# Optimization experiments

Hardware: AMD Instinct MI355X
Metric: run time of the kernel (lower is better)

Reference implementation:

```python
import jax, jax.numpy as jnp
import numpy as np

NUM_HEADS = 4
SPATIAL_DS = 2
EPS = 1e-5


def setup_inputs() -> dict:
    key = jax.random.key(0)
    ks = jax.random.split(key, 6)
    B, C, H, W = 8, 256, 64, 64
    hd = C // NUM_HEADS
    return {
        "x": jax.random.normal(ks[0], (B, C, H, W), jnp.float32),
        "gn_w": jnp.ones((C,), jnp.float32),
        "gn_b": jnp.zeros((C,), jnp.float32),
        "wq": jax.random.normal(ks[1], (C, C), jnp.float32) * (C ** -0.5),
        "wk": jax.random.normal(ks[2], (hd, C), jnp.float32) * (C ** -0.5),
        "wv": jax.random.normal(ks[3], (hd, C), jnp.float32) * (C ** -0.5),
        "wo": jax.random.normal(ks[4], (C, C), jnp.float32) * (C ** -0.5),
        "gamma": jnp.full((C,), 1e-4, jnp.float32),
    }


def reference(x, gn_w, gn_b, wq, wk, wv, wo, gamma):
    B, C, H, W = x.shape
    hd = C // NUM_HEADS
    scale = hd ** -0.5
    ds = SPATIAL_DS

    # GroupNorm with 1 group: normalize over (C,H,W) per sample, per-channel affine
    mu = jnp.mean(x, axis=(1, 2, 3), keepdims=True)
    var = jnp.var(x, axis=(1, 2, 3), keepdims=True)
    xn = (x - mu) * jax.lax.rsqrt(var + EPS)
    xn = xn * gn_w[None, :, None, None] + gn_b[None, :, None, None]

    # Q projection (1x1 conv == channel matmul): (B, heads, N, hd)
    q = jnp.einsum('oc,bchw->bohw', wq, xn).reshape(B, NUM_HEADS, hd, H * W)
    q = jnp.swapaxes(q, 2, 3)  # (B, h, N, hd)

    # AvgPool2d(ds, ds) on normalized input for K/V
    Hd, Wd = H // ds, W // ds
    x_ds = xn.reshape(B, C, Hd, ds, Wd, ds).mean(axis=(3, 5))

    k = jnp.einsum('oc,bchw->bohw', wk, x_ds).reshape(B, hd, Hd * Wd)
    k = jnp.swapaxes(k, 1, 2)  # (B, M, hd) single shared head
    v = jnp.einsum('oc,bchw->bohw', wv, x_ds).reshape(B, hd, Hd * Wd)
    v = jnp.swapaxes(v, 1, 2)  # (B, M, hd)

    # Multi-query attention: queries per-head, shared K/V
    attn = jnp.einsum('bhnd,bmd->bhnm', q, k) * scale
    attn = jax.nn.softmax(attn, axis=-1)
    out = jnp.einsum('bhnm,bmd->bhnd', attn, v)  # (B, h, N, hd)

    out = jnp.swapaxes(out, 2, 3).reshape(B, C, H, W)
    out = jnp.einsum('oc,bchw->bohw', wo, out)

    return x + out * gamma[None, :, None, None]
```

## Files before the change

kernel.cpp:

```cpp
#include <hip/hip_runtime.h>


#define CNT_INV (1.0f/1048576.0f)
#define EPSV 1e-5f
#define QSCALE 0.18033688f

#define WS_STATS 0
#define WS_XNT   64
#define WS_XDS   4194368
#define WS_K     5242944
#define WS_V     5505088
#define WS_WQB   5767232
#define WS_WKV   5800000
#define WS_WOB   5816384

typedef __attribute__((ext_vector_type(8))) short bf8_t;
typedef __attribute__((ext_vector_type(4))) float f4_t;

static __device__ __forceinline__ unsigned fbits(float f) {
  union { float f; unsigned u; } v; v.f = f; return v.u;
}
static __device__ __forceinline__ unsigned short f2bf(float f) {
  unsigned u = fbits(f);
  return (unsigned short)((u + 0x7fffu + ((u >> 16) & 1u)) >> 16);
}
static __device__ __forceinline__ unsigned pk_rnd(float a, float b) {
  return __builtin_amdgcn_perm(fbits(b) + 0x8000u, fbits(a) + 0x8000u, 0x07060302u);
}
static __device__ __forceinline__ unsigned pk_tr(float a, float b) {
  return __builtin_amdgcn_perm(fbits(b), fbits(a), 0x07060302u);
}
static __device__ __forceinline__ float bf2f(unsigned short h) {
  union { unsigned u; float f; } v; v.u = ((unsigned)h) << 16; return v.f;
}
static __device__ __forceinline__ float fexp2(float x) {
  float r; asm("v_exp_f32 %0, %1" : "=v"(r) : "v"(x)); return r;
}

__global__ __launch_bounds__(256) void k_prep_stats(const float* __restrict__ x,
                                                    const float* __restrict__ wq,
                                                    const float* __restrict__ wk,
                                                    const float* __restrict__ wv,
                                                    const float* __restrict__ wo,
                                                    float* __restrict__ stats,
                                                    unsigned short* __restrict__ wqb,
                                                    unsigned short* __restrict__ wkvb,
                                                    unsigned short* __restrict__ wob) {
  const int blk = blockIdx.x;
  const int t = threadIdx.x;
  if (blk < 512) {
    const int b = blk >> 6;
    const int chunk = blk & 63;
    const float4* xb = (const float4*)(x + (size_t)b * 1048576 + (size_t)chunk * 16384);
    float s = 0.f, s2 = 0.f;
#pragma unroll
    for (int it = 0; it < 16; ++it) {
      float4 v = xb[it * 256 + t];
      s  += v.x + v.y + v.z + v.w;
      s2 += v.x * v.x + v.y * v.y + v.z * v.z + v.w * v.w;
    }
#pragma unroll
    for (int o = 32; o > 0; o >>= 1) {
      s  += __shfl_down(s, o);
      s2 += __shfl_down(s2, o);
    }
    __shared__ float red[8];
    const int wid = t >> 6;
    if ((t & 63) == 0) { red[wid] = s; red[4 + wid] = s2; }
    __syncthreads();
    if (t == 0) {
      atomicAdd(&stats[b * 2 + 0], red[0] + red[1] + red[2] + red[3]);
      atomicAdd(&stats[b * 2 + 1], red[4] + red[5] + red[6] + red[7]);
    }
  } else {
    const int idx = (blk - 512) * 256 + t;
    if (idx < 65536) wqb[idx] = f2bf(wq[idx]);
    else if (idx < 81920) wkvb[idx - 65536] = f2bf(wk[idx - 65536]);
    else if (idx < 98304) wkvb[idx - 65536] = f2bf(wv[idx - 81920]);
    else if (idx < 163840) wob[idx - 98304] = f2bf(wo[idx - 98304]);
  }
}

__global__ __launch_bounds__(256) void k_xnt(const float* __restrict__ x,
                                             const float* __restrict__ gnw,
                                             const float* __restrict__ gnb,
                                             const float* __restrict__ stats,
                                             unsigned short* __restrict__ xnT,
                                             unsigned short* __restrict__ xdsT) {
  __shared__ unsigned short T[128][72];
  const int t = threadIdx.x;
  const int b = blockIdx.z, c0 = blockIdx.y * 64, hp = blockIdx.x;
  const int n0 = hp * 128;
  const float mu = stats[b * 2 + 0] * CNT_INV;
  const float rstd = rsqrtf(stats[b * 2 + 1] * CNT_INV - mu * mu + EPSV);
  const int n4 = (t & 31) * 4, cl = t >> 5;
  const int wswz = t & 7;
#pragma unroll
  for (int p = 0; p < 8; ++p) {
    const int c = c0 + p * 8 + cl;
    const float gw = gnw[c] * rstd;
    const float gb = gnb[c] - mu * rstd * gnw[c];
    const int pc = (p ^ wswz) * 8 + cl;
    float4 v = *(const float4*)&x[(size_t)(b * 256 + c) * 4096 + n0 + n4];
    T[n4 + 0][pc] = f2bf(v.x * gw + gb);
    T[n4 + 1][pc] = f2bf(v.y * gw + gb);
    T[n4 + 2][pc] = f2bf(v.z * gw + gb);
    T[n4 + 3][pc] = f2bf(v.w * gw + gb);
  }
  __syncthreads();
  {
    const int r = t >> 1, cb4 = (t & 1) * 4;
    const int rswz = (t >> 3) & 7;
    unsigned short* dst = xnT + ((size_t)b * 4096 + n0 + r) * 256 + c0 + cb4 * 8;
#pragma unroll
    for (int u = 0; u < 4; ++u)
      *(uint4*)(dst + u * 8) = *(const uint4*)&T[r][((cb4 + u) ^ rswz) * 8];
  }
  {
    const int wd = t >> 3, c8 = t & 7;
    const int pswz = (wd >> 1) & 7;
    const int pc = (c8 ^ pswz) * 8;
    uint4 u0 = *(const uint4*)&T[2 * wd][pc];
    uint4 u1 = *(const uint4*)&T[2 * wd + 1][pc];
    uint4 u2 = *(const uint4*)&T[64 + 2 * wd][pc];
    uint4 u3 = *(const uint4*)&T[64 + 2 * wd + 1][pc];
    const unsigned* p0 = (const unsigned*)&u0; const unsigned* p1 = (const unsigned*)&u1;
    const unsigned* p2 = (const unsigned*)&u2; const unsigned* p3 = (const unsigned*)&u3;
    unsigned outp[4];
#pragma unroll
    for (int i = 0; i < 4; ++i) {
      float lo = (bf2f((unsigned short)p0[i]) + bf2f((unsigned short)p1[i]) +
                  bf2f((unsigned short)p2[i]) + bf2f((unsigned short)p3[i])) * 0.25f;
      float hi = (bf2f((unsigned short)(p0[i] >> 16)) + bf2f((unsigned short)(p1[i] >> 16)) +
                  bf2f((unsigned short)(p2[i] >> 16)) + bf2f((unsigned short)(p3[i] >> 16))) * 0.25f;
      outp[i] = pk_rnd(lo, hi);
    }
    *(uint4*)(xdsT + ((size_t)b * 1024 + hp * 32 + wd) * 256 + c0 + c8 * 8) = *(uint4*)outp;
  }
}

__global__ __launch_bounds__(256) void k_gemm_kv(const unsigned short* __restrict__ wkvb,
                                                 const unsigned short* __restrict__ xdsT,
                                                 unsigned short* __restrict__ kbf,
                                                 unsigned short* __restrict__ vtbf) {
  __shared__ __align__(16) unsigned short kv[2][64][72];
  const int t = threadIdx.x;
  const int w = t >> 6, l = t & 63, lane16 = l & 15, quad = l >> 4;
  const int m0 = blockIdx.x * 64, b = blockIdx.y;
  const unsigned short* Abase = wkvb + (size_t)(w * 32 + lane16) * 256 + quad * 8;
  const unsigned short* Bbase = xdsT + ((size_t)b * 1024 + m0 + lane16) * 256 + quad * 8;
  f4_t acc[2][4];
#pragma unroll
  for (int i = 0; i < 2; ++i)
#pragma unroll
    for (int j = 0; j < 4; ++j) acc[i][j] = (f4_t){0.f, 0.f, 0.f, 0.f};
  bf8_t Ac[2], Bc[4];
#pragma unroll
  for (int og = 0; og < 2; ++og) Ac[og] = *(const bf8_t*)(Abase + (size_t)og * 16 * 256);
#pragma unroll
  for (int mg = 0; mg < 4; ++mg) Bc[mg] = *(const bf8_t*)(Bbase + (size_t)mg * 16 * 256);
  for (int kc = 0; kc < 256; kc += 32) {
    const int kn = (kc + 32) & 255;
    bf8_t An[2], Bn[4];
#pragma unroll
    for (int og = 0; og < 2; ++og) An[og] = *(const bf8_t*)(Abase + (size_t)og * 16 * 256 + kn);
#pragma unroll
    for (int mg = 0; mg < 4; ++mg) Bn[mg] = *(const bf8_t*)(Bbase + (size_t)mg * 16 * 256 + kn);
#pragma unroll
    for (int og = 0; og < 2; ++og)
#pragma unroll
      for (int mg = 0; mg < 4; ++mg)
        acc[og][mg] = __builtin_amdgcn_mfma_f32_16x16x32_bf16(Ac[og], Bc[mg], acc[og][mg], 0, 0, 0);
#pragma unroll
    for (int og = 0; og < 2; ++og) Ac[og] = An[og];
#pragma unroll
    for (int mg = 0; mg < 4; ++mg) Bc[mg] = Bn[mg];
  }
  if (w < 2) {
#pragma unroll
    for (int og = 0; og < 2; ++og)
#pragma unroll
      for (int mg = 0; mg < 4; ++mg) {
        uint2 p;
        p.x = pk_rnd(acc[og][mg][0], acc[og][mg][1]);
        p.y = pk_rnd(acc[og][mg][2], acc[og][mg][3]);
        *(uint2*)&kv[0][mg * 16 + lane16][w * 32 + og * 16 + quad * 4] = p;
      }
  } else {
#pragma unroll
    for (int og = 0; og < 2; ++og)
#pragma unroll
      for (int mg = 0; mg < 4; ++mg) {
        const int d0 = (w - 2) * 32 + og * 16 + quad * 4;
#pragma unroll
        for (int r = 0; r < 4; ++r)
          kv[1][d0 + r][mg * 16 + lane16] = f2bf(acc[og][mg][r]);
      }
  }
  __syncthreads();
  {
    const int row = t >> 2, q2 = t & 3;
    const int e = row & 7;
    uint4 k0 = *(const uint4*)&kv[0][row][q2 * 16];
    uint4 k1 = *(const uint4*)&kv[0][row][q2 * 16 + 8];
    unsigned short* kd = kbf + (size_t)b * 65536 + (size_t)(m0 + row) * 64;
    *(uint4*)(kd + ((q2 * 2) ^ e) * 8)     = k0;
    *(uint4*)(kd + ((q2 * 2 + 1) ^ e) * 8) = k1;
    uint4 v0 = *(const uint4*)&kv[1][row][q2 * 16];
    uint4 v1 = *(const uint4*)&kv[1][row][q2 * 16 + 8];
    unsigned short* vd = vtbf + (size_t)b * 65536 + (size_t)(blockIdx.x * 2 + (q2 >> 1)) * 2048 +
                         (size_t)row * 32 + (q2 & 1) * 16;
    *(uint4*)vd = v0; *(uint4*)(vd + 8) = v1;
  }
}

__global__ __launch_bounds__(256) void k_fused(const unsigned short* __restrict__ wqb,
                                               const unsigned short* __restrict__ xnT,
                                               const unsigned short* __restrict__ kbf,
                                               const unsigned short* __restrict__ vtbf,
                                               const unsigned short* __restrict__ wob,
                                               const float* __restrict__ x,
                                               const float* __restrict__ gamma,
                                               float* __restrict__ outp) {
  __shared__ __align__(16) unsigned short smem[20480];
  __shared__ __align__(16) unsigned short kst[2][2048];
  __shared__ __align__(16) unsigned short vst[2][2048];
  const int t = threadIdx.x;
  const int w = t >> 6, l = t & 63, lane16 = l & 15, quad = l >> 4;
  const int n0 = blockIdx.x * 64, b = blockIdx.y;
  const int h = w;
  unsigned short* qst = smem + w * 4608;
  unsigned short (*plds)[64][40] = (unsigned short (*)[64][40])(smem + w * 5120);
  unsigned short (*aos)[264] = (unsigned short (*)[264])smem;

  const int sw = w & 1;
  const unsigned short* sbase = (w < 2) ? (kbf + (size_t)b * 65536) : (vtbf + (size_t)b * 65536);
  unsigned short* sdst0 = ((w < 2) ? &kst[0][0] : &vst[0][0]) + sw * 1024 + l * 8;
  unsigned short* sdst1 = ((w < 2) ? &kst[1][0] : &vst[1][0]) + sw * 1024 + l * 8;

#define STAGE_ISSUE(WIN, R0, R1)                                              \
  { const unsigned short* sp = sbase + (size_t)(WIN) * 2048 + sw * 1024 + l * 8; \
    R0 = *(const uint4*)sp; R1 = *(const uint4*)(sp + 512); }
#define STAGE_WRITE(DP, R0, R1)                                               \
  { *(uint4*)(DP) = R0; *(uint4*)((DP) + 512) = R1; }

#define READ_K(BUF, KREG)                                                     \
  {                                                                           \
    _Pragma("unroll")                                                         \
    for (int s = 0; s < 2; ++s) {                                             \
      _Pragma("unroll")                                                       \
      for (int dc = 0; dc < 2; ++dc)                                          \
        KREG[s][dc] = *(const bf8_t*)&kst[BUF][(s * 16 + lane16) * 64 +       \
                                              (((dc * 4 + quad) ^ (lane16 & 7)) * 8)]; \
    }                                                                         \
  }
#define READ_V(BUF, VREG)                                                     \
  {                                                                           \
    _Pragma("unroll")                                                         \
    for (int dg = 0; dg < 4; ++dg)                                            \
      VREG[dg] = *(const bf8_t*)&vst[BUF][(dg * 16 + lane16) * 32 + quad * 8]; \
  }

  const unsigned short* kb = kbf;

  {
    const unsigned short* Abase = wqb + (size_t)(h * 64 + lane16) * 256 + quad * 8;
    const unsigned short* Bbase = xnT + ((size_t)b * 4096 + n0 + lane16) * 256 + quad * 8;
    f4_t qacc[4][4];
#pragma unroll
    for (int i = 0; i < 4; ++i)
#pragma unroll
      for (int j = 0; j < 4; ++j) qacc[i][j] = (f4_t){0.f, 0.f, 0.f, 0.f};
    for (int kc = 0; kc < 256; kc += 32) {
      bf8_t A[4], Bf[4];
#pragma unroll
      for (int og = 0; og < 4; ++og) A[og] = *(const bf8_t*)(Abase + (size_t)og * 16 * 256 + kc);
#pragma unroll
      for (int ng = 0; ng < 4; ++ng) Bf[ng] = *(const bf8_t*)(Bbase + (size_t)ng * 16 * 256 + kc);
#pragma unroll
      for (int og = 0; og < 4; ++og)
#pragma unroll
        for (int ng = 0; ng < 4; ++ng)
          qacc[og][ng] = __builtin_amdgcn_mfma_f32_16x16x32_bf16(A[og], Bf[ng], qacc[og][ng], 0, 0, 0);
    }
#pragma unroll
    for (int og = 0; og < 4; ++og)
#pragma unroll
      for (int ng = 0; ng < 4; ++ng) {
        uint2 p;
        p.x = pk_rnd(qacc[og][ng][0] * QSCALE, qacc[og][ng][1] * QSCALE);
        p.y = pk_rnd(qacc[og][ng][2] * QSCALE, qacc[og][ng][3] * QSCALE);
        *(uint2*)&qst[(ng * 16 + lane16) * 72 + og * 16 + quad * 4] = p;
      }
  }
  bf8_t Qf[4][2];
#pragma unroll
  for (int qg = 0; qg < 4; ++qg)
#pragma unroll
    for (int dc = 0; dc < 2; ++dc)
      Qf[qg][dc] = *(const bf8_t*)&qst[(qg * 16 + lane16) * 72 + dc * 32 + quad * 8];
  __syncthreads();

  f4_t O[4][4];
#pragma unroll
  for (int dg = 0; dg < 4; ++dg)
#pragma unroll
    for (int qg = 0; qg < 4; ++qg) O[dg][qg] = (f4_t){0.f, 0.f, 0.f, 0.f};
  f4_t O4[4];
#pragma unroll
  for (int qg = 0; qg < 4; ++qg) O4[qg] = (f4_t){0.f, 0.f, 0.f, 0.f};
  const short onebf = (lane16 == 0) ? (short)0x3F80 : (short)0;
  const bf8_t Aone = {onebf, onebf, onebf, onebf, onebf, onebf, onebf, onebf};

#define SSTEP(KREG, BUF)                                                      \
  {                                                                           \
    _Pragma("unroll")                                                         \
    for (int qg = 0; qg < 4; ++qg) {                                          \
      _Pragma("unroll")                                                       \
      for (int s = 0; s < 2; ++s) {                                           \
        f4_t S = (f4_t){0.f, 0.f, 0.f, 0.f};                                  \
        S = __builtin_amdgcn_mfma_f32_16x16x32_bf16(KREG[s][0], Qf[qg][0], S, 0, 0, 0); \
        S = __builtin_amdgcn_mfma_f32_16x16x32_bf16(KREG[s][1], Qf[qg][1], S, 0, 0, 0); \
        float e0 = fexp2(S[0]);                                               \
        float e1 = fexp2(S[1]);                                               \
        float e2 = fexp2(S[2]);                                               \
        float e3 = fexp2(S[3]);                                               \
        uint2 p; p.x = pk_tr(e0, e1); p.y = pk_tr(e2, e3);                    \
        *(uint2*)&plds[BUF][qg * 16 + lane16][s * 16 + quad * 4] = p;         \
      }                                                                       \
    }                                                                         \
  }

  {
    uint4 a0, a1, b0, b1;
    STAGE_ISSUE(0, a0, a1);
    STAGE_ISSUE(1, b0, b1);
    STAGE_WRITE(sdst0, a0, a1);
    STAGE_WRITE(sdst1, b0, b1);
  }
  __syncthreads();

  bf8_t Kc[2][2], Vc[4];
  READ_K(0, Kc);
  SSTEP(Kc, 0);
  READ_V(0, Vc);
  __syncthreads();

  for (int it = 1; it < 32; ++it) {
    const int cur = it & 1, pb = cur ^ 1;
    uint4 g0, g1;
    if (it < 31) STAGE_ISSUE(it + 1, g0, g1);
    bf8_t Pf[4];
#pragma unroll
    for (int qg = 0; qg < 4; ++qg)
      Pf[qg] = *(const bf8_t*)&plds[pb][qg * 16 + lane16][quad * 8];
    READ_K(cur, Kc);
    bf8_t Vn[4];
    READ_V(cur, Vn);
    __builtin_amdgcn_s_setprio(1);
#pragma unroll
    for (int dg = 0; dg < 4; ++dg)
#pragma unroll
      for (int qg = 0; qg < 4; ++qg)
        O[dg][qg] = __builtin_amdgcn_mfma_f32_16x16x32_bf16(Vc[dg], Pf[qg], O[dg][qg], 0, 0, 0);
#pragma unroll
    for (int qg = 0; qg < 4; ++qg)
      O4[qg] = __builtin_amdgcn_mfma_f32_16x16x32_bf16(Aone, Pf[qg], O4[qg], 0, 0, 0);
    __builtin_amdgcn_s_setprio(0);
    SSTEP(Kc, cur);
#pragma unroll
    for (int dg = 0; dg < 4; ++dg) Vc[dg] = Vn[dg];
    if (it < 31) STAGE_WRITE((cur ? sdst0 : sdst1), g0, g1);
    __syncthreads();
  }
  {
    bf8_t Pf[4];
#pragma unroll
    for (int qg = 0; qg < 4; ++qg)
      Pf[qg] = *(const bf8_t*)&plds[1][qg * 16 + lane16][quad * 8];
    __builtin_amdgcn_s_setprio(1);
#pragma unroll
    for (int dg = 0; dg < 4; ++dg)
#pragma unroll
      for (int qg = 0; qg < 4; ++qg)
        O[dg][qg] = __builtin_amdgcn_mfma_f32_16x16x32_bf16(Vc[dg], Pf[qg], O[dg][qg], 0, 0, 0);
#pragma unroll
    for (int qg = 0; qg < 4; ++qg)
      O4[qg] = __builtin_amdgcn_mfma_f32_16x16x32_bf16(Aone, Pf[qg], O4[qg], 0, 0, 0);
    __builtin_amdgcn_s_setprio(0);
  }
#undef SSTEP
#undef STAGE_ISSUE
#undef STAGE_WRITE
#undef READ_K
#undef READ_V
  (void)kb;

  float rden[4];
#pragma unroll
  for (int qg = 0; qg < 4; ++qg) {
    float d = __shfl(O4[qg][0], lane16);
    rden[qg] = 1.f / d;
  }

  __syncthreads();
#pragma unroll
  for (int dg = 0; dg < 4; ++dg)
#pragma unroll
    for (int qg = 0; qg < 4; ++qg) {
      const int c0 = h * 64 + dg * 16 + quad * 4;
      uint2 p;
      p.x = pk_rnd(O[dg][qg][0] * rden[qg], O[dg][qg][1] * rden[qg]);
      p.y = pk_rnd(O[dg][qg][2] * rden[qg], O[dg][qg][3] * rden[qg]);
      *(uint2*)&aos[qg * 16 + lane16][c0] = p;
    }
  __syncthreads();

  {
    const unsigned short* Wbase = wob + (size_t)(w * 64 + lane16) * 256 + quad * 8;
    f4_t acc[4][4];
#pragma unroll
    for (int i = 0; i < 4; ++i)
#pragma unroll
      for (int j = 0; j < 4; ++j) acc[i][j] = (f4_t){0.f, 0.f, 0.f, 0.f};
    for (int kc = 0; kc < 256; kc += 32) {
      bf8_t A[4], Bf[4];
#pragma unroll
      for (int og = 0; og < 4; ++og) A[og] = *(const bf8_t*)(Wbase + (size_t)og * 16 * 256 + kc);
#pragma unroll
      for (int ng = 0; ng < 4; ++ng) Bf[ng] = *(const bf8_t*)&aos[ng * 16 + lane16][kc + quad * 8];
#pragma unroll
      for (int og = 0; og < 4; ++og)
#pragma unroll
        for (int ng = 0; ng < 4; ++ng)
          acc[og][ng] = __builtin_amdgcn_mfma_f32_16x16x32_bf16(A[og], Bf[ng], acc[og][ng], 0, 0, 0);
    }
#pragma unroll
    for (int og = 0; og < 4; ++og) {
      float4 g4 = *(const float4*)&gamma[w * 64 + og * 16 + quad * 4];
      const float g[4] = {g4.x, g4.y, g4.z, g4.w};
#pragma unroll
      for (int ng = 0; ng < 4; ++ng) {
        const int n = n0 + ng * 16 + lane16;
#pragma unroll
        for (int r = 0; r < 4; ++r) {
          const int o = w * 64 + og * 16 + quad * 4 + r;
          const size_t ix = ((size_t)(b * 256 + o)) * 4096 + n;
          outp[ix] = x[ix] + g[r] * acc[og][ng][r];
        }
      }
    }
  }
}

extern "C" void kernel_launch(void* const* d_in, const int* in_sizes, int n_in,
                              void* d_out, int out_size, void* d_ws, size_t ws_size,
                              hipStream_t stream) {
  const float* x     = (const float*)d_in[0];
  const float* gnw   = (const float*)d_in[1];
  const float* gnb   = (const float*)d_in[2];
  const float* wq    = (const float*)d_in[3];
  const float* wk    = (const float*)d_in[4];
  const float* wv    = (const float*)d_in[5];
  const float* wo    = (const float*)d_in[6];
  const float* gamma = (const float*)d_in[7];
  float* out = (float*)d_out;
  float* ws  = (float*)d_ws;
  unsigned short* xnT  = (unsigned short*)(ws + WS_XNT);
  unsigned short* xdsT = (unsigned short*)(ws + WS_XDS);
  unsigned short* kbf  = (unsigned short*)(ws + WS_K);
  unsigned short* vtbf = (unsigned short*)(ws + WS_V);
  unsigned short* wqb  = (unsigned short*)(ws + WS_WQB);
  unsigned short* wkvb = (unsigned short*)(ws + WS_WKV);
  unsigned short* wob  = (unsigned short*)(ws + WS_WOB);

  hipMemsetAsync(ws, 0, 256, stream);
  k_prep_stats<<<1152, 256, 0, stream>>>(x, wq, wk, wv, wo, ws + WS_STATS, wqb, wkvb, wob);
  k_xnt<<<dim3(32, 4, 8), 256, 0, stream>>>(x, gnw, gnb, ws + WS_STATS, xnT, xdsT);
  k_gemm_kv<<<dim3(16, 8), 256, 0, stream>>>(wkvb, xdsT, kbf, vtbf);
  k_fused<<<dim3(64, 8), 256, 0, stream>>>(wqb, xnT, kbf, vtbf, wob, x, gamma, out);
}
```

Before: 194.1 us.

## Split fused attention KV range across two wave groups with 512-thread blocks

The fused attention kernel now runs 8 waves per block. Two groups of four waves each handle half of the 1024 key/value positions for the same 64 queries, and the partial numerators and denominators are combined through shared memory before the output projection. The Q projection and the output projection are split across both groups as well. The software-pipelined softmax step (compute P for the next window while consuming the previous one) is replaced by a simpler sequential per-window loop, and the KV GEMM drops its register prefetch. This raises wave-level parallelism and shortens each wave's serial loop, at the cost of extra barriers, a shared-memory reduction and a less overlapped inner loop.

```diff
diff --git a/kernel.cpp b/kernel.cpp
--- a/kernel.cpp
+++ b/kernel.cpp
@@ -126,16 +126,16 @@
     uint4 u3 = *(const uint4*)&T[64 + 2 * wd + 1][pc];
     const unsigned* p0 = (const unsigned*)&u0; const unsigned* p1 = (const unsigned*)&u1;
     const unsigned* p2 = (const unsigned*)&u2; const unsigned* p3 = (const unsigned*)&u3;
-    unsigned outp[4];
+    unsigned outv[4];
 #pragma unroll
     for (int i = 0; i < 4; ++i) {
       float lo = (bf2f((unsigned short)p0[i]) + bf2f((unsigned short)p1[i]) +
                   bf2f((unsigned short)p2[i]) + bf2f((unsigned short)p3[i])) * 0.25f;
       float hi = (bf2f((unsigned short)(p0[i] >> 16)) + bf2f((unsigned short)(p1[i] >> 16)) +
                   bf2f((unsigned short)(p2[i] >> 16)) + bf2f((unsigned short)(p3[i] >> 16))) * 0.25f;
-      outp[i] = pk_rnd(lo, hi);
-    }
-    *(uint4*)(xdsT + ((size_t)b * 1024 + hp * 32 + wd) * 256 + c0 + c8 * 8) = *(uint4*)outp;
+      outv[i] = pk_rnd(lo, hi);
+    }
+    *(uint4*)(xdsT + ((size_t)b * 1024 + hp * 32 + wd) * 256 + c0 + c8 * 8) = *(uint4*)outv;
   }
 }
 
@@ -154,27 +154,17 @@
   for (int i = 0; i < 2; ++i)
 #pragma unroll
     for (int j = 0; j < 4; ++j) acc[i][j] = (f4_t){0.f, 0.f, 0.f, 0.f};
-  bf8_t Ac[2], Bc[4];
-#pragma unroll
-  for (int og = 0; og < 2; ++og) Ac[og] = *(const bf8_t*)(Abase + (size_t)og * 16 * 256);
-#pragma unroll
-  for (int mg = 0; mg < 4; ++mg) Bc[mg] = *(const bf8_t*)(Bbase + (size_t)mg * 16 * 256);
   for (int kc = 0; kc < 256; kc += 32) {
-    const int kn = (kc + 32) & 255;
-    bf8_t An[2], Bn[4];
-#pragma unroll
-    for (int og = 0; og < 2; ++og) An[og] = *(const bf8_t*)(Abase + (size_t)og * 16 * 256 + kn);
-#pragma unroll
-    for (int mg = 0; mg < 4; ++mg) Bn[mg] = *(const bf8_t*)(Bbase + (size_t)mg * 16 * 256 + kn);
+    bf8_t A[2], Bf[4];
+#pragma unroll
+    for (int og = 0; og < 2; ++og) A[og] = *(const bf8_t*)(Abase + (size_t)og * 16 * 256 + kc);
+#pragma unroll
+    for (int mg = 0; mg < 4; ++mg) Bf[mg] = *(const bf8_t*)(Bbase + (size_t)mg * 16 * 256 + kc);
 #pragma unroll
     for (int og = 0; og < 2; ++og)
 #pragma unroll
       for (int mg = 0; mg < 4; ++mg)
-        acc[og][mg] = __builtin_amdgcn_mfma_f32_16x16x32_bf16(Ac[og], Bc[mg], acc[og][mg], 0, 0, 0);
-#pragma unroll
-    for (int og = 0; og < 2; ++og) Ac[og] = An[og];
-#pragma unroll
-    for (int mg = 0; mg < 4; ++mg) Bc[mg] = Bn[mg];
+        acc[og][mg] = __builtin_amdgcn_mfma_f32_16x16x32_bf16(A[og], Bf[mg], acc[og][mg], 0, 0, 0);
   }
   if (w < 2) {
 #pragma unroll
@@ -214,43 +204,84 @@
   }
 }
 
-__global__ __launch_bounds__(256) void k_fused(const unsigned short* __restrict__ wqb,
-                                               const unsigned short* __restrict__ xnT,
-                                               const unsigned short* __restrict__ kbf,
-                                               const unsigned short* __restrict__ vtbf,
-                                               const unsigned short* __restrict__ wob,
-                                               const float* __restrict__ x,
-                                               const float* __restrict__ gamma,
-                                               float* __restrict__ outp) {
-  __shared__ __align__(16) unsigned short smem[20480];
-  __shared__ __align__(16) unsigned short kst[2][2048];
-  __shared__ __align__(16) unsigned short vst[2][2048];
+__global__ __launch_bounds__(512, 4) void k_fused(const unsigned short* __restrict__ wqb,
+                                                  const unsigned short* __restrict__ xnT,
+                                                  const unsigned short* __restrict__ kbf,
+                                                  const unsigned short* __restrict__ vtbf,
+                                                  const unsigned short* __restrict__ wob,
+                                                  const float* __restrict__ x,
+                                                  const float* __restrict__ gamma,
+                                                  float* __restrict__ outp) {
+  __shared__ __align__(16) unsigned short smem[18432];
+  __shared__ __align__(16) unsigned short kstA[2][2][2048];
+  __shared__ __align__(16) unsigned short vstA[2][2][2048];
   const int t = threadIdx.x;
   const int w = t >> 6, l = t & 63, lane16 = l & 15, quad = l >> 4;
+  const int h = w & 3, kvg = w >> 2;
   const int n0 = blockIdx.x * 64, b = blockIdx.y;
-  const int h = w;
-  unsigned short* qst = smem + w * 4608;
-  unsigned short (*plds)[64][40] = (unsigned short (*)[64][40])(smem + w * 5120);
+  unsigned short* qst = smem + h * 4608;
+  unsigned short (*plds)[36] = (unsigned short (*)[36])(smem + w * 2304);
   unsigned short (*aos)[264] = (unsigned short (*)[264])smem;
 
-  const int sw = w & 1;
-  const unsigned short* sbase = (w < 2) ? (kbf + (size_t)b * 65536) : (vtbf + (size_t)b * 65536);
-  unsigned short* sdst0 = ((w < 2) ? &kst[0][0] : &vst[0][0]) + sw * 1024 + l * 8;
-  unsigned short* sdst1 = ((w < 2) ? &kst[1][0] : &vst[1][0]) + sw * 1024 + l * 8;
+  const unsigned short* kb = kbf + (size_t)b * 65536;
+  const unsigned short* vb = vtbf + (size_t)b * 65536;
+
+  {
+    const unsigned short* Abase = wqb + (size_t)(h * 64 + lane16) * 256 + quad * 8;
+    const unsigned short* Bbase = xnT + ((size_t)b * 4096 + n0 + kvg * 32 + lane16) * 256 + quad * 8;
+    f4_t qacc[4][2];
+#pragma unroll
+    for (int i = 0; i < 4; ++i)
+#pragma unroll
+      for (int j = 0; j < 2; ++j) qacc[i][j] = (f4_t){0.f, 0.f, 0.f, 0.f};
+    for (int kc = 0; kc < 256; kc += 32) {
+      bf8_t A[4], Bf[2];
+#pragma unroll
+      for (int og = 0; og < 4; ++og) A[og] = *(const bf8_t*)(Abase + (size_t)og * 16 * 256 + kc);
+#pragma unroll
+      for (int j = 0; j < 2; ++j) Bf[j] = *(const bf8_t*)(Bbase + (size_t)j * 16 * 256 + kc);
+#pragma unroll
+      for (int og = 0; og < 4; ++og)
+#pragma unroll
+        for (int j = 0; j < 2; ++j)
+          qacc[og][j] = __builtin_amdgcn_mfma_f32_16x16x32_bf16(A[og], Bf[j], qacc[og][j], 0, 0, 0);
+    }
+#pragma unroll
+    for (int og = 0; og < 4; ++og)
+#pragma unroll
+      for (int j = 0; j < 2; ++j) {
+        const int ng = kvg * 2 + j;
+        uint2 p;
+        p.x = pk_rnd(qacc[og][j][0] * QSCALE, qacc[og][j][1] * QSCALE);
+        p.y = pk_rnd(qacc[og][j][2] * QSCALE, qacc[og][j][3] * QSCALE);
+        *(uint2*)&qst[(ng * 16 + lane16) * 72 + og * 16 + quad * 4] = p;
+      }
+  }
+  __syncthreads();
+  bf8_t Qf[4][2];
+#pragma unroll
+  for (int qg = 0; qg < 4; ++qg)
+#pragma unroll
+    for (int dc = 0; dc < 2; ++dc)
+      Qf[qg][dc] = *(const bf8_t*)&qst[(qg * 16 + lane16) * 72 + dc * 32 + quad * 8];
+
+  const int wr = w & 3, sw = wr & 1;
+  const unsigned short* sbase = (wr < 2) ? kb : vb;
+  unsigned short* sdst0 = ((wr < 2) ? &kstA[kvg][0][0] : &vstA[kvg][0][0]) + sw * 1024 + l * 8;
+  unsigned short* sdst1 = ((wr < 2) ? &kstA[kvg][1][0] : &vstA[kvg][1][0]) + sw * 1024 + l * 8;
 
 #define STAGE_ISSUE(WIN, R0, R1)                                              \
   { const unsigned short* sp = sbase + (size_t)(WIN) * 2048 + sw * 1024 + l * 8; \
     R0 = *(const uint4*)sp; R1 = *(const uint4*)(sp + 512); }
 #define STAGE_WRITE(DP, R0, R1)                                               \
   { *(uint4*)(DP) = R0; *(uint4*)((DP) + 512) = R1; }
-
 #define READ_K(BUF, KREG)                                                     \
   {                                                                           \
     _Pragma("unroll")                                                         \
     for (int s = 0; s < 2; ++s) {                                             \
       _Pragma("unroll")                                                       \
       for (int dc = 0; dc < 2; ++dc)                                          \
-        KREG[s][dc] = *(const bf8_t*)&kst[BUF][(s * 16 + lane16) * 64 +       \
+        KREG[s][dc] = *(const bf8_t*)&kstA[kvg][BUF][(s * 16 + lane16) * 64 + \
                                               (((dc * 4 + quad) ^ (lane16 & 7)) * 8)]; \
     }                                                                         \
   }
@@ -258,47 +289,14 @@
   {                                                                           \
     _Pragma("unroll")                                                         \
     for (int dg = 0; dg < 4; ++dg)                                            \
-      VREG[dg] = *(const bf8_t*)&vst[BUF][(dg * 16 + lane16) * 32 + quad * 8]; \
-  }
-
-  const unsigned short* kb = kbf;
-
-  {
-    const unsigned short* Abase = wqb + (size_t)(h * 64 + lane16) * 256 + quad * 8;
-    const unsigned short* Bbase = xnT + ((size_t)b * 4096 + n0 + lane16) * 256 + quad * 8;
-    f4_t qacc[4][4];
-#pragma unroll
-    for (int i = 0; i < 4; ++i)
-#pragma unroll
-      for (int j = 0; j < 4; ++j) qacc[i][j] = (f4_t){0.f, 0.f, 0.f, 0.f};
-    for (int kc = 0; kc < 256; kc += 32) {
-      bf8_t A[4], Bf[4];
-#pragma unroll
-      for (int og = 0; og < 4; ++og) A[og] = *(const bf8_t*)(Abase + (size_t)og * 16 * 256 + kc);
-#pragma unroll
-      for (int ng = 0; ng < 4; ++ng) Bf[ng] = *(const bf8_t*)(Bbase + (size_t)ng * 16 * 256 + kc);
-#pragma unroll
-      for (int og = 0; og < 4; ++og)
-#pragma unroll
-        for (int ng = 0; ng < 4; ++ng)
-          qacc[og][ng] = __builtin_amdgcn_mfma_f32_16x16x32_bf16(A[og], Bf[ng], qacc[og][ng], 0, 0, 0);
-    }
-#pragma unroll
-    for (int og = 0; og < 4; ++og)
-#pragma unroll
-      for (int ng = 0; ng < 4; ++ng) {
-        uint2 p;
-        p.x = pk_rnd(qacc[og][ng][0] * QSCALE, qacc[og][ng][1] * QSCALE);
-        p.y = pk_rnd(qacc[og][ng][2] * QSCALE, qacc[og][ng][3] * QSCALE);
-        *(uint2*)&qst[(ng * 16 + lane16) * 72 + og * 16 + quad * 4] = p;
-      }
-  }
-  bf8_t Qf[4][2];
-#pragma unroll
-  for (int qg = 0; qg < 4; ++qg)
-#pragma unroll
-    for (int dc = 0; dc < 2; ++dc)
-      Qf[qg][dc] = *(const bf8_t*)&qst[(qg * 16 + lane16) * 72 + dc * 32 + quad * 8];
+      VREG[dg] = *(const bf8_t*)&vstA[kvg][BUF][(dg * 16 + lane16) * 32 + quad * 8]; \
+  }
+
+  {
+    uint4 a0, a1;
+    STAGE_ISSUE(kvg * 16, a0, a1);
+    STAGE_WRITE(sdst0, a0, a1);
+  }
   __syncthreads();
 
   f4_t O[4][4];
@@ -312,51 +310,33 @@
   const short onebf = (lane16 == 0) ? (short)0x3F80 : (short)0;
   const bf8_t Aone = {onebf, onebf, onebf, onebf, onebf, onebf, onebf, onebf};
 
-#define SSTEP(KREG, BUF)                                                      \
-  {                                                                           \
-    _Pragma("unroll")                                                         \
-    for (int qg = 0; qg < 4; ++qg) {                                          \
-      _Pragma("unroll")                                                       \
-      for (int s = 0; s < 2; ++s) {                                           \
-        f4_t S = (f4_t){0.f, 0.f, 0.f, 0.f};                                  \
-        S = __builtin_amdgcn_mfma_f32_16x16x32_bf16(KREG[s][0], Qf[qg][0], S, 0, 0, 0); \
-        S = __builtin_amdgcn_mfma_f32_16x16x32_bf16(KREG[s][1], Qf[qg][1], S, 0, 0, 0); \
-        float e0 = fexp2(S[0]);                                               \
-        float e1 = fexp2(S[1]);                                               \
-        float e2 = fexp2(S[2]);                                               \
-        float e3 = fexp2(S[3]);                                               \
-        uint2 p; p.x = pk_tr(e0, e1); p.y = pk_tr(e2, e3);                    \
-        *(uint2*)&plds[BUF][qg * 16 + lane16][s * 16 + quad * 4] = p;         \
-      }                                                                       \
-    }                                                                         \
-  }
-
-  {
-    uint4 a0, a1, b0, b1;
-    STAGE_ISSUE(0, a0, a1);
-    STAGE_ISSUE(1, b0, b1);
-    STAGE_WRITE(sdst0, a0, a1);
-    STAGE_WRITE(sdst1, b0, b1);
-  }
-  __syncthreads();
-
-  bf8_t Kc[2][2], Vc[4];
-  READ_K(0, Kc);
-  SSTEP(Kc, 0);
-  READ_V(0, Vc);
-  __syncthreads();
-
-  for (int it = 1; it < 32; ++it) {
-    const int cur = it & 1, pb = cur ^ 1;
+  for (int it = 0; it < 16; ++it) {
+    const int cur = it & 1;
     uint4 g0, g1;
-    if (it < 31) STAGE_ISSUE(it + 1, g0, g1);
+    if (it < 15) STAGE_ISSUE(kvg * 16 + it + 1, g0, g1);
+    bf8_t Kc[2][2];
+    READ_K(cur, Kc);
+#pragma unroll
+    for (int qg = 0; qg < 4; ++qg) {
+#pragma unroll
+      for (int s = 0; s < 2; ++s) {
+        f4_t S = (f4_t){0.f, 0.f, 0.f, 0.f};
+        S = __builtin_amdgcn_mfma_f32_16x16x32_bf16(Kc[s][0], Qf[qg][0], S, 0, 0, 0);
+        S = __builtin_amdgcn_mfma_f32_16x16x32_bf16(Kc[s][1], Qf[qg][1], S, 0, 0, 0);
+        float e0 = fexp2(S[0]);
+        float e1 = fexp2(S[1]);
+        float e2 = fexp2(S[2]);
+        float e3 = fexp2(S[3]);
+        uint2 p; p.x = pk_tr(e0, e1); p.y = pk_tr(e2, e3);
+        *(uint2*)&plds[qg * 16 + lane16][s * 16 + quad * 4] = p;
+      }
+    }
+    bf8_t Vc[4];
+    READ_V(cur, Vc);
     bf8_t Pf[4];
 #pragma unroll
     for (int qg = 0; qg < 4; ++qg)
-      Pf[qg] = *(const bf8_t*)&plds[pb][qg * 16 + lane16][quad * 8];
-    READ_K(cur, Kc);
-    bf8_t Vn[4];
-    READ_V(cur, Vn);
+      Pf[qg] = *(const bf8_t*)&plds[qg * 16 + lane16][quad * 8];
     __builtin_amdgcn_s_setprio(1);
 #pragma unroll
     for (int dg = 0; dg < 4; ++dg)
@@ -367,84 +347,100 @@
     for (int qg = 0; qg < 4; ++qg)
       O4[qg] = __builtin_amdgcn_mfma_f32_16x16x32_bf16(Aone, Pf[qg], O4[qg], 0, 0, 0);
     __builtin_amdgcn_s_setprio(0);
-    SSTEP(Kc, cur);
-#pragma unroll
-    for (int dg = 0; dg < 4; ++dg) Vc[dg] = Vn[dg];
-    if (it < 31) STAGE_WRITE((cur ? sdst0 : sdst1), g0, g1);
+    if (it < 15) STAGE_WRITE((cur ? sdst0 : sdst1), g0, g1);
     __syncthreads();
   }
-  {
-    bf8_t Pf[4];
-#pragma unroll
-    for (int qg = 0; qg < 4; ++qg)
-      Pf[qg] = *(const bf8_t*)&plds[1][qg * 16 + lane16][quad * 8];
-    __builtin_amdgcn_s_setprio(1);
-#pragma unroll
-    for (int dg = 0; dg < 4; ++dg)
-#pragma unroll
-      for (int qg = 0; qg < 4; ++qg)
-        O[dg][qg] = __builtin_amdgcn_mfma_f32_16x16x32_bf16(Vc[dg], Pf[qg], O[dg][qg], 0, 0, 0);
-#pragma unroll
-    for (int qg = 0; qg < 4; ++qg)
-      O4[qg] = __builtin_amdgcn_mfma_f32_16x16x32_bf16(Aone, Pf[qg], O4[qg], 0, 0, 0);
-    __builtin_amdgcn_s_setprio(0);
-  }
-#undef SSTEP
 #undef STAGE_ISSUE
 #undef STAGE_WRITE
 #undef READ_K
 #undef READ_V
-  (void)kb;
-
-  float rden[4];
-#pragma unroll
-  for (int qg = 0; qg < 4; ++qg) {
-    float d = __shfl(O4[qg][0], lane16);
-    rden[qg] = 1.f / d;
-  }
-
-  __syncthreads();
-#pragma unroll
-  for (int dg = 0; dg < 4; ++dg)
+
+  float* fcomb = (float*)&kstA[0][0][0];
+#pragma unroll
+  for (int dgr = 0; dgr < 4; ++dgr) {
+    if (kvg == 1) {
+#pragma unroll
+      for (int qg = 0; qg < 4; ++qg)
+#pragma unroll
+        for (int rr = 0; rr < 4; ++rr)
+          fcomb[(qg * 4 + rr) * 256 + h * 64 + l] = O[dgr][qg][rr];
+    }
+    __syncthreads();
+    if (kvg == 0) {
+#pragma unroll
+      for (int qg = 0; qg < 4; ++qg)
+#pragma unroll
+        for (int rr = 0; rr < 4; ++rr)
+          O[dgr][qg][rr] += fcomb[(qg * 4 + rr) * 256 + h * 64 + l];
+    }
+    __syncthreads();
+  }
+  if (kvg == 1) {
+#pragma unroll
+    for (int qg = 0; qg < 4; ++qg)
+#pragma unroll
+      for (int rr = 0; rr < 4; ++rr)
+        fcomb[(qg * 4 + rr) * 256 + h * 64 + l] = O4[qg][rr];
+  }
+  __syncthreads();
+  if (kvg == 0) {
+#pragma unroll
+    for (int qg = 0; qg < 4; ++qg)
+#pragma unroll
+      for (int rr = 0; rr < 4; ++rr)
+        O4[qg][rr] += fcomb[(qg * 4 + rr) * 256 + h * 64 + l];
+  }
+  __syncthreads();
+
+  if (kvg == 0) {
+    float rden[4];
 #pragma unroll
     for (int qg = 0; qg < 4; ++qg) {
-      const int c0 = h * 64 + dg * 16 + quad * 4;
-      uint2 p;
-      p.x = pk_rnd(O[dg][qg][0] * rden[qg], O[dg][qg][1] * rden[qg]);
-      p.y = pk_rnd(O[dg][qg][2] * rden[qg], O[dg][qg][3] * rden[qg]);
-      *(uint2*)&aos[qg * 16 + lane16][c0] = p;
-    }
-  __syncthreads();
-
-  {
-    const unsigned short* Wbase = wob + (size_t)(w * 64 + lane16) * 256 + quad * 8;
-    f4_t acc[4][4];
-#pragma unroll
-    for (int i = 0; i < 4; ++i)
+      float d = __shfl(O4[qg][0], lane16);
+      rden[qg] = 1.f / d;
+    }
+#pragma unroll
+    for (int dg = 0; dg < 4; ++dg)
+#pragma unroll
+      for (int qg = 0; qg < 4; ++qg) {
+        const int c0 = h * 64 + dg * 16 + quad * 4;
+        uint2 p;
+        p.x = pk_rnd(O[dg][qg][0] * rden[qg], O[dg][qg][1] * rden[qg]);
+        p.y = pk_rnd(O[dg][qg][2] * rden[qg], O[dg][qg][3] * rden[qg]);
+        *(uint2*)&aos[qg * 16 + lane16][c0] = p;
+      }
+  }
+  __syncthreads();
+
+  {
+    const unsigned short* Wbase = wob + (size_t)(w * 32 + lane16) * 256 + quad * 8;
+    f4_t acc[2][4];
+#pragma unroll
+    for (int i = 0; i < 2; ++i)
 #pragma unroll
       for (int j = 0; j < 4; ++j) acc[i][j] = (f4_t){0.f, 0.f, 0.f, 0.f};
     for (int kc = 0; kc < 256; kc += 32) {
-      bf8_t A[4], Bf[4];
-#pragma unroll
-      for (int og = 0; og < 4; ++og) A[og] = *(const bf8_t*)(Wbase + (size_t)og * 16 * 256 + kc);
+      bf8_t A[2], Bf[4];
+#pragma unroll
+      for (int og = 0; og < 2; ++og) A[og] = *(const bf8_t*)(Wbase + (size_t)og * 16 * 256 + kc);
 #pragma unroll
       for (int ng = 0; ng < 4; ++ng) Bf[ng] = *(const bf8_t*)&aos[ng * 16 + lane16][kc + quad * 8];
 #pragma unroll
-      for (int og = 0; og < 4; ++og)
+      for (int og = 0; og < 2; ++og)
 #pragma unroll
         for (int ng = 0; ng < 4; ++ng)
           acc[og][ng] = __builtin_amdgcn_mfma_f32_16x16x32_bf16(A[og], Bf[ng], acc[og][ng], 0, 0, 0);
     }
 #pragma unroll
-    for (int og = 0; og < 4; ++og) {
-      float4 g4 = *(const float4*)&gamma[w * 64 + og * 16 + quad * 4];
+    for (int og = 0; og < 2; ++og) {
+      float4 g4 = *(const float4*)&gamma[w * 32 + og * 16 + quad * 4];
       const float g[4] = {g4.x, g4.y, g4.z, g4.w};
 #pragma unroll
       for (int ng = 0; ng < 4; ++ng) {
         const int n = n0 + ng * 16 + lane16;
 #pragma unroll
         for (int r = 0; r < 4; ++r) {
-          const int o = w * 64 + og * 16 + quad * 4 + r;
+          const int o = w * 32 + og * 16 + quad * 4 + r;
           const size_t ix = ((size_t)(b * 256 + o)) * 4096 + n;
           outp[ix] = x[ix] + g[r] * acc[og][ng][r];
         }
@@ -478,5 +474,5 @@
   k_prep_stats<<<1152, 256, 0, stream>>>(x, wq, wk, wv, wo, ws + WS_STATS, wqb, wkvb, wob);
   k_xnt<<<dim3(32, 4, 8), 256, 0, stream>>>(x, gnw, gnb, ws + WS_STATS, xnT, xdsT);
   k_gemm_kv<<<dim3(16, 8), 256, 0, stream>>>(wkvb, xdsT, kbf, vtbf);
-  k_fused<<<dim3(64, 8), 256, 0, stream>>>(wqb, xnT, kbf, vtbf, wob, x, gamma, out);
-}
+  k_fused<<<dim3(64, 8), 512, 0, stream>>>(wqb, xnT, kbf, vtbf, wob, x, gamma, out);
+}
```

Result: slower. 277.1 us (+42.8%).
